# Kernel optimization log

Hardware: AMD Instinct MI355X
Metric: run time of the kernel (lower is better)

Reference implementation:

```python
import jax, jax.numpy as jnp
import numpy as np

TOP_K_FREQ = 16


def setup_inputs() -> dict:
    key = jax.random.key(0)
    x = jax.random.normal(key, (64, 4096, 128), dtype=jnp.float32)
    return {"x": x}


def reference(x):
    B, L, C = x.shape
    freq = jnp.fft.rfft(x, axis=1)              # [B, F, C] complex, F = L//2 + 1
    F = freq.shape[1]
    k = min(TOP_K_FREQ, F)
    mag = jnp.abs(freq)                          # [B, F, C]
    # top-k over frequency axis, vectorized across (B, C)
    mag_bcf = jnp.transpose(mag, (0, 2, 1))      # [B, C, F]
    _, idx = jax.lax.top_k(mag_bcf, k)           # idx: [B, C, k]
    b_ix = jnp.arange(B)[:, None, None]
    c_ix = jnp.arange(C)[None, :, None]
    mask_bcf = jnp.zeros((B, C, F), dtype=x.dtype).at[b_ix, c_ix, idx].set(1.0)
    mask = jnp.transpose(mask_bcf, (0, 2, 1))    # [B, F, C]
    freq_filtered = freq * mask
    out = jnp.fft.irfft(freq_filtered, n=L, axis=1)  # [B, L, C]
    return out.astype(x.dtype)
```

## Files before the change

kernel.cpp:

```cpp
#include <hip/hip_runtime.h>


#define SWZ(i) ((i) ^ (((i) >> 4) & 15))

__device__ __forceinline__ int drev16(int x) {
  return ((x & 15) << 8) | (x & 0xF0) | ((x >> 8) & 15);
}

__device__ __forceinline__ float2 cmulf(float2 a, float c, float s) {
  return make_float2(a.x * c - a.y * s, a.x * s + a.y * c);
}

__device__ __forceinline__ void bfly4(float2& a0, float2& a1, float2& a2, float2& a3) {
  float ar = a0.x + a2.x, ai = a0.y + a2.y;
  float br = a0.x - a2.x, bi = a0.y - a2.y;
  float cr = a1.x + a3.x, ci = a1.y + a3.y;
  float dr = a1.x - a3.x, di = a1.y - a3.y;
  a0 = make_float2(ar + cr, ai + ci);
  a1 = make_float2(br + di, bi - dr);
  a2 = make_float2(ar - cr, ai - ci);
  a3 = make_float2(br - di, bi + dr);
}

__device__ __forceinline__ void dft16(float2* v) {
  const float C16[10] = {1.f, 0.9238795325112867f, 0.7071067811865476f, 0.3826834323650898f, 0.f,
                         -0.3826834323650898f, -0.7071067811865476f, -0.9238795325112867f, -1.f,
                         -0.9238795325112867f};
  const float S16[10] = {0.f, -0.3826834323650898f, -0.7071067811865476f, -0.9238795325112867f, -1.f,
                         -0.9238795325112867f, -0.7071067811865476f, -0.3826834323650898f, 0.f,
                         0.3826834323650898f};
  #pragma unroll
  for (int j2 = 0; j2 < 4; j2++) {
    bfly4(v[j2], v[j2 + 4], v[j2 + 8], v[j2 + 12]);
    if (j2 > 0) {
      v[j2 + 4]  = cmulf(v[j2 + 4],  C16[j2],     S16[j2]);
      v[j2 + 8]  = cmulf(v[j2 + 8],  C16[2 * j2], S16[2 * j2]);
      v[j2 + 12] = cmulf(v[j2 + 12], C16[3 * j2], S16[3 * j2]);
    }
  }
  #pragma unroll
  for (int r2 = 0; r2 < 4; r2++) bfly4(v[4 * r2], v[4 * r2 + 1], v[4 * r2 + 2], v[4 * r2 + 3]);
}

template <int STRIDE, int M>
__device__ __forceinline__ void fft_pass(float2* Zl, int base, int j) {
  const int kRev4[16] = {0, 4, 8, 12, 1, 5, 9, 13, 2, 6, 10, 14, 3, 7, 11, 15};
  float2 v[16];
  #pragma unroll
  for (int p = 0; p < 16; p++) v[p] = Zl[SWZ(base + j + STRIDE * p)];
  dft16(v);
  #pragma unroll
  for (int r = 0; r < 16; r++) {
    float2 u = v[kRev4[r]];
    if (M > 0 && r > 0) {
      int a = (j * r) & (M - 1);
      float x = (float)a * (1.0f / (float)M);
      float s = -__builtin_amdgcn_sinf(x);
      float c =  __builtin_amdgcn_cosf(x);
      u = cmulf(u, c, s);
    }
    Zl[SWZ(base + j + STRIDE * r)] = u;
  }
}


__global__ __launch_bounds__(256, 4) void fourier_fused(
    const float2* __restrict__ X2, float2* __restrict__ O2) {
  __shared__ float2 Z[4096];
  __shared__ float4 CF[32];
  __shared__ float  CFf[32];

  const int tid = threadIdx.x;
  const int o = ((blockIdx.x & 7) << 9) + (blockIdx.x >> 3);
  const int b = o >> 6;
  const int q = o & 63;

  const float2* src = X2 + (size_t)b * 4096 * 64 + q;
  #pragma unroll
  for (int k = 0; k < 16; k++) {
    int l = tid + 256 * k;
    Z[SWZ(l)] = src[(size_t)l * 64];
  }
  __syncthreads();

  fft_pass<256, 4096>(Z, 0, tid);
  __syncthreads();
  fft_pass<16, 256>(Z, (tid >> 4) << 8, tid & 15);
  __syncthreads();
  fft_pass<1, 0>(Z, tid << 4, 0);
  __syncthreads();

  const int wv = tid >> 6;
  const int lane = tid & 63;

  if (wv < 2) {
    const int ch = wv;
    int rF = 0; float rA = 0.f, rB = 0.f;
    float m2[32];
    #pragma unroll
    for (int k = 0; k < 32; k++) {
      int f = lane + (k << 6);
      float2 P = Z[SWZ(drev16(f))];
      float2 Q = Z[SWZ(drev16((4096 - f) & 4095))];
      float xr = ch ? (P.y + Q.y) : (P.x + Q.x);
      float xi = ch ? (Q.x - P.x) : (P.y - Q.y);
      m2[k] = xr * xr + xi * xi;
    }
    float m2x = -1.f;
    if (lane == 0) {
      float2 P = Z[SWZ(8)];
      float t = ch ? P.y : P.x;
      m2x = 4.f * t * t;
    }
    for (int r = 0; r < 16; r++) {
      float bv = -1e30f; int bf = 0;
      #pragma unroll
      for (int k = 0; k < 32; k++) {
        int f = lane + (k << 6);
        if (m2[k] > bv) { bv = m2[k]; bf = f; }
      }
      if (m2x > bv) { bv = m2x; bf = 2048; }
      #pragma unroll
      for (int off = 32; off; off >>= 1) {
        float ov = __shfl_down(bv, off);
        int   of = __shfl_down(bf, off);
        if (ov > bv || (ov == bv && of < bf)) { bv = ov; bf = of; }
      }
      bf = __shfl(bf, 0);
      if (lane == r) {
        rF = bf;
        float2 P = Z[SWZ(drev16(bf))];
        float2 Q = Z[SWZ(drev16((4096 - bf) & 4095))];
        rA = ch ? 0.5f * (P.y + Q.y) : 0.5f * (P.x + Q.x);
        rB = ch ? 0.5f * (Q.x - P.x) : 0.5f * (P.y - Q.y);
      }
      if (bf == 2048) {
        if (lane == 0) m2x = -2.f;
      } else if ((bf & 63) == lane) {
        int kk = bf >> 6;
        #pragma unroll
        for (int k = 0; k < 32; k++) if (k == kk) m2[k] = -2.f;
      }
    }

    if (lane < 16) {
      const float inv = 2.44140625e-4f;
      float w = (rF == 0 || rF == 2048) ? inv : 2.f * inv;
      float fv = (float)rF;
      float dx = fv * 0.0625f;
      dx -= floorf(dx);
      float cd = __builtin_amdgcn_cosf(dx);
      float sd = __builtin_amdgcn_sinf(dx);
      CF[ch * 16 + lane] = make_float4(w * rA, -w * rB, cd, sd);
      CFf[ch * 16 + lane] = fv;
    }
  }
  __syncthreads();

  float* S = (float*)Z;
  const float tf = (float)tid;
  #pragma unroll
  for (int cc = 0; cc < 2; cc++) {
    float u[16], v[16], T[16];
    #pragma unroll
    for (int j = 0; j < 16; j++) {
      float4 cf = CF[cc * 16 + j];
      float f  = CFf[cc * 16 + j];
      float x0 = f * tf * 2.44140625e-4f;
      x0 -= floorf(x0);
      float c0 = __builtin_amdgcn_cosf(x0);
      float s0 = __builtin_amdgcn_sinf(x0);
      float G = fmaf(cf.x, c0, cf.y * s0);
      float H = fmaf(cf.y, c0, -cf.x * s0);
      u[j] = G;
      v[j] = fmaf(G, cf.z, -H * cf.w);
      T[j] = cf.z + cf.z;
    }
    #pragma unroll
    for (int k = 0; k < 16; k += 2) {
      float s0a = 0.f, s1a = 0.f;
      #pragma unroll
      for (int j = 0; j < 16; j++) {
        s0a += u[j];
        v[j] = fmaf(T[j], u[j], -v[j]);
      }
      #pragma unroll
      for (int j = 0; j < 16; j++) {
        s1a += v[j];
        u[j] = fmaf(T[j], v[j], -u[j]);
      }
      S[cc * 4096 + tid + 256 * k]       = s0a;
      S[cc * 4096 + tid + 256 * (k + 1)] = s1a;
    }
  }

  float2* dst = O2 + (size_t)b * 4096 * 64 + q;
  #pragma unroll
  for (int k = 0; k < 16; k++) {
    int l = tid + 256 * k;
    dst[(size_t)l * 64] = make_float2(S[l], S[4096 + l]);
  }
}

extern "C" void kernel_launch(void* const* d_in, const int* in_sizes, int n_in,
                              void* d_out, int out_size, void* d_ws, size_t ws_size,
                              hipStream_t stream) {
  (void)in_sizes; (void)n_in; (void)ws_size; (void)out_size; (void)d_ws;
  const float2* x = (const float2*)d_in[0];
  float2* out = (float2*)d_out;

  fourier_fused<<<dim3(64 * 64), dim3(256), 0, stream>>>(x, out);
}
```

Measured before the change: 504.7 us.

## Switch to radix-8 FFT with 512 threads per block

Replaces the three-pass radix-16 in-LDS FFT with four radix-8 passes and doubles the block size to 512 threads. Each thread now holds 8 instead of 16 complex values, which lowers register pressure and raises the number of waves resident to hide global-memory latency. The twiddle phase, bit-reversal indexing and synthesis stride are updated to match. It adds one extra LDS pass and barrier per block and more threads idle during the two-wave top-k section.

```diff
diff --git a/kernel.cpp b/kernel.cpp
--- a/kernel.cpp
+++ b/kernel.cpp
@@ -3,68 +3,69 @@
 
 #define SWZ(i) ((i) ^ (((i) >> 4) & 15))
 
-__device__ __forceinline__ int drev16(int x) {
-  return ((x & 15) << 8) | (x & 0xF0) | ((x >> 8) & 15);
+__device__ __forceinline__ int drev8(int x) {
+  return ((x & 7) << 9) | ((x & 0x38) << 3) | ((x >> 3) & 0x38) | ((x >> 9) & 7);
 }
 
 __device__ __forceinline__ float2 cmulf(float2 a, float c, float s) {
   return make_float2(a.x * c - a.y * s, a.x * s + a.y * c);
 }
 
-__device__ __forceinline__ void bfly4(float2& a0, float2& a1, float2& a2, float2& a3) {
-  float ar = a0.x + a2.x, ai = a0.y + a2.y;
-  float br = a0.x - a2.x, bi = a0.y - a2.y;
-  float cr = a1.x + a3.x, ci = a1.y + a3.y;
-  float dr = a1.x - a3.x, di = a1.y - a3.y;
-  a0 = make_float2(ar + cr, ai + ci);
-  a1 = make_float2(br + di, bi - dr);
-  a2 = make_float2(ar - cr, ai - ci);
-  a3 = make_float2(br - di, bi + dr);
-}
-
-__device__ __forceinline__ void dft16(float2* v) {
-  const float C16[10] = {1.f, 0.9238795325112867f, 0.7071067811865476f, 0.3826834323650898f, 0.f,
-                         -0.3826834323650898f, -0.7071067811865476f, -0.9238795325112867f, -1.f,
-                         -0.9238795325112867f};
-  const float S16[10] = {0.f, -0.3826834323650898f, -0.7071067811865476f, -0.9238795325112867f, -1.f,
-                         -0.9238795325112867f, -0.7071067811865476f, -0.3826834323650898f, 0.f,
-                         0.3826834323650898f};
-  #pragma unroll
-  for (int j2 = 0; j2 < 4; j2++) {
-    bfly4(v[j2], v[j2 + 4], v[j2 + 8], v[j2 + 12]);
-    if (j2 > 0) {
-      v[j2 + 4]  = cmulf(v[j2 + 4],  C16[j2],     S16[j2]);
-      v[j2 + 8]  = cmulf(v[j2 + 8],  C16[2 * j2], S16[2 * j2]);
-      v[j2 + 12] = cmulf(v[j2 + 12], C16[3 * j2], S16[3 * j2]);
-    }
-  }
-  #pragma unroll
-  for (int r2 = 0; r2 < 4; r2++) bfly4(v[4 * r2], v[4 * r2 + 1], v[4 * r2 + 2], v[4 * r2 + 3]);
+__device__ __forceinline__ float2 cadd(float2 a, float2 b) { return make_float2(a.x + b.x, a.y + b.y); }
+__device__ __forceinline__ float2 csub(float2 a, float2 b) { return make_float2(a.x - b.x, a.y - b.y); }
+__device__ __forceinline__ float2 cmulnegi(float2 a) { return make_float2(a.y, -a.x); }
+__device__ __forceinline__ float2 cmulposi(float2 a) { return make_float2(-a.y, a.x); }
+
+__device__ __forceinline__ void dft8(float2* a) {
+  const float R = 0.7071067811865476f;
+  float2 t0 = cadd(a[0], a[4]), t1 = cadd(a[1], a[5]);
+  float2 t2 = cadd(a[2], a[6]), t3 = cadd(a[3], a[7]);
+  float2 u0 = csub(a[0], a[4]);
+  float2 d1 = csub(a[1], a[5]);
+  float2 u1 = make_float2(R * (d1.x + d1.y), R * (d1.y - d1.x));
+  float2 u2 = cmulnegi(csub(a[2], a[6]));
+  float2 d3 = csub(a[3], a[7]);
+  float2 u3 = make_float2(R * (d3.y - d3.x), R * (-(d3.x + d3.y)));
+  {
+    float2 b0 = cadd(t0, t2), b1 = csub(t0, t2);
+    float2 b2 = cadd(t1, t3), b3 = csub(t1, t3);
+    a[0] = cadd(b0, b2);
+    a[2] = cadd(b1, cmulnegi(b3));
+    a[4] = csub(b0, b2);
+    a[6] = cadd(b1, cmulposi(b3));
+  }
+  {
+    float2 b0 = cadd(u0, u2), b1 = csub(u0, u2);
+    float2 b2 = cadd(u1, u3), b3 = csub(u1, u3);
+    a[1] = cadd(b0, b2);
+    a[3] = cadd(b1, cmulnegi(b3));
+    a[5] = csub(b0, b2);
+    a[7] = cadd(b1, cmulposi(b3));
+  }
 }
 
 template <int STRIDE, int M>
-__device__ __forceinline__ void fft_pass(float2* Zl, int base, int j) {
-  const int kRev4[16] = {0, 4, 8, 12, 1, 5, 9, 13, 2, 6, 10, 14, 3, 7, 11, 15};
-  float2 v[16];
-  #pragma unroll
-  for (int p = 0; p < 16; p++) v[p] = Zl[SWZ(base + j + STRIDE * p)];
-  dft16(v);
-  #pragma unroll
-  for (int r = 0; r < 16; r++) {
-    float2 u = v[kRev4[r]];
-    if (M > 0 && r > 0) {
-      int a = (j * r) & (M - 1);
+__device__ __forceinline__ void fft_pass8(float2* Zl, int base, int j) {
+  float2 v[8];
+  #pragma unroll
+  for (int p = 0; p < 8; p++) v[p] = Zl[SWZ(base + j + STRIDE * p)];
+  dft8(v);
+  #pragma unroll
+  for (int r = 1; r < 8; r++) {
+    if (M > 8) {
+      int a = j * r;
       float x = (float)a * (1.0f / (float)M);
       float s = -__builtin_amdgcn_sinf(x);
       float c =  __builtin_amdgcn_cosf(x);
-      u = cmulf(u, c, s);
-    }
-    Zl[SWZ(base + j + STRIDE * r)] = u;
-  }
-}
-
-
-__global__ __launch_bounds__(256, 4) void fourier_fused(
+      v[r] = cmulf(v[r], c, s);
+    }
+  }
+  #pragma unroll
+  for (int r = 0; r < 8; r++) Zl[SWZ(base + j + STRIDE * r)] = v[r];
+}
+
+
+__global__ __launch_bounds__(512, 8) void fourier_fused(
     const float2* __restrict__ X2, float2* __restrict__ O2) {
   __shared__ float2 Z[4096];
   __shared__ float4 CF[32];
@@ -77,17 +78,19 @@
 
   const float2* src = X2 + (size_t)b * 4096 * 64 + q;
   #pragma unroll
-  for (int k = 0; k < 16; k++) {
-    int l = tid + 256 * k;
+  for (int k = 0; k < 8; k++) {
+    int l = tid + 512 * k;
     Z[SWZ(l)] = src[(size_t)l * 64];
   }
   __syncthreads();
 
-  fft_pass<256, 4096>(Z, 0, tid);
-  __syncthreads();
-  fft_pass<16, 256>(Z, (tid >> 4) << 8, tid & 15);
-  __syncthreads();
-  fft_pass<1, 0>(Z, tid << 4, 0);
+  fft_pass8<512, 4096>(Z, 0, tid);
+  __syncthreads();
+  fft_pass8<64, 512>(Z, (tid >> 6) << 9, tid & 63);
+  __syncthreads();
+  fft_pass8<8, 64>(Z, (tid >> 3) << 6, tid & 7);
+  __syncthreads();
+  fft_pass8<1, 8>(Z, tid << 3, 0);
   __syncthreads();
 
   const int wv = tid >> 6;
@@ -100,15 +103,15 @@
     #pragma unroll
     for (int k = 0; k < 32; k++) {
       int f = lane + (k << 6);
-      float2 P = Z[SWZ(drev16(f))];
-      float2 Q = Z[SWZ(drev16((4096 - f) & 4095))];
+      float2 P = Z[SWZ(drev8(f))];
+      float2 Q = Z[SWZ(drev8((4096 - f) & 4095))];
       float xr = ch ? (P.y + Q.y) : (P.x + Q.x);
       float xi = ch ? (Q.x - P.x) : (P.y - Q.y);
       m2[k] = xr * xr + xi * xi;
     }
     float m2x = -1.f;
     if (lane == 0) {
-      float2 P = Z[SWZ(8)];
+      float2 P = Z[SWZ(4)];
       float t = ch ? P.y : P.x;
       m2x = 4.f * t * t;
     }
@@ -129,8 +132,8 @@
       bf = __shfl(bf, 0);
       if (lane == r) {
         rF = bf;
-        float2 P = Z[SWZ(drev16(bf))];
-        float2 Q = Z[SWZ(drev16((4096 - bf) & 4095))];
+        float2 P = Z[SWZ(drev8(bf))];
+        float2 Q = Z[SWZ(drev8((4096 - bf) & 4095))];
         rA = ch ? 0.5f * (P.y + Q.y) : 0.5f * (P.x + Q.x);
         rB = ch ? 0.5f * (Q.x - P.x) : 0.5f * (P.y - Q.y);
       }
@@ -147,7 +150,7 @@
       const float inv = 2.44140625e-4f;
       float w = (rF == 0 || rF == 2048) ? inv : 2.f * inv;
       float fv = (float)rF;
-      float dx = fv * 0.0625f;
+      float dx = fv * 0.125f;
       dx -= floorf(dx);
       float cd = __builtin_amdgcn_cosf(dx);
       float sd = __builtin_amdgcn_sinf(dx);
@@ -177,7 +180,7 @@
       T[j] = cf.z + cf.z;
     }
     #pragma unroll
-    for (int k = 0; k < 16; k += 2) {
+    for (int k = 0; k < 8; k += 2) {
       float s0a = 0.f, s1a = 0.f;
       #pragma unroll
       for (int j = 0; j < 16; j++) {
@@ -189,15 +192,15 @@
         s1a += v[j];
         u[j] = fmaf(T[j], v[j], -u[j]);
       }
-      S[cc * 4096 + tid + 256 * k]       = s0a;
-      S[cc * 4096 + tid + 256 * (k + 1)] = s1a;
+      S[cc * 4096 + tid + 512 * k]       = s0a;
+      S[cc * 4096 + tid + 512 * (k + 1)] = s1a;
     }
   }
 
   float2* dst = O2 + (size_t)b * 4096 * 64 + q;
   #pragma unroll
-  for (int k = 0; k < 16; k++) {
-    int l = tid + 256 * k;
+  for (int k = 0; k < 8; k++) {
+    int l = tid + 512 * k;
     dst[(size_t)l * 64] = make_float2(S[l], S[4096 + l]);
   }
 }
@@ -209,5 +212,5 @@
   const float2* x = (const float2*)d_in[0];
   float2* out = (float2*)d_out;
 
-  fourier_fused<<<dim3(64 * 64), dim3(256), 0, stream>>>(x, out);
-}
+  fourier_fused<<<dim3(64 * 64), dim3(512), 0, stream>>>(x, out);
+}
```

New measurement: 596.0 us. 1.18x slower.

## Process four channels per block with float4 global loads and stores

Applied to the files above, without the earlier changes.

Each block now handles four channels instead of two. It loads them as float4 and runs two sequential packed-complex FFT and top-k passes, keeping the second pair in registers. The synthesis step is restructured into grouped chunks accumulating 16 outputs, and the results are written back as float4. The intent is wider, better-coalesced global accesses and half as many blocks. The cost is more registers and serialized work per block, which may reduce occupancy.

```diff
diff --git a/kernel.cpp b/kernel.cpp
--- a/kernel.cpp
+++ b/kernel.cpp
@@ -63,109 +63,17 @@
   }
 }
 
-
-__global__ __launch_bounds__(256, 4) void fourier_fused(
-    const float2* __restrict__ X2, float2* __restrict__ O2) {
-  __shared__ float2 Z[4096];
-  __shared__ float4 CF[32];
-  __shared__ float  CFf[32];
-
-  const int tid = threadIdx.x;
-  const int o = ((blockIdx.x & 7) << 9) + (blockIdx.x >> 3);
-  const int b = o >> 6;
-  const int q = o & 63;
-
-  const float2* src = X2 + (size_t)b * 4096 * 64 + q;
-  #pragma unroll
-  for (int k = 0; k < 16; k++) {
-    int l = tid + 256 * k;
-    Z[SWZ(l)] = src[(size_t)l * 64];
-  }
-  __syncthreads();
-
-  fft_pass<256, 4096>(Z, 0, tid);
-  __syncthreads();
-  fft_pass<16, 256>(Z, (tid >> 4) << 8, tid & 15);
-  __syncthreads();
-  fft_pass<1, 0>(Z, tid << 4, 0);
-  __syncthreads();
-
-  const int wv = tid >> 6;
-  const int lane = tid & 63;
-
-  if (wv < 2) {
-    const int ch = wv;
-    int rF = 0; float rA = 0.f, rB = 0.f;
-    float m2[32];
+__device__ __forceinline__ void synthc(const float4* CF, const float* CFf,
+                                       int cbase, float tf, float* acc) {
+  #pragma unroll
+  for (int k = 0; k < 16; k++) acc[k] = 0.f;
+  #pragma unroll 1
+  for (int g = 0; g < 4; g++) {
+    float u[4], v[4], T[4];
     #pragma unroll
-    for (int k = 0; k < 32; k++) {
-      int f = lane + (k << 6);
-      float2 P = Z[SWZ(drev16(f))];
-      float2 Q = Z[SWZ(drev16((4096 - f) & 4095))];
-      float xr = ch ? (P.y + Q.y) : (P.x + Q.x);
-      float xi = ch ? (Q.x - P.x) : (P.y - Q.y);
-      m2[k] = xr * xr + xi * xi;
-    }
-    float m2x = -1.f;
-    if (lane == 0) {
-      float2 P = Z[SWZ(8)];
-      float t = ch ? P.y : P.x;
-      m2x = 4.f * t * t;
-    }
-    for (int r = 0; r < 16; r++) {
-      float bv = -1e30f; int bf = 0;
-      #pragma unroll
-      for (int k = 0; k < 32; k++) {
-        int f = lane + (k << 6);
-        if (m2[k] > bv) { bv = m2[k]; bf = f; }
-      }
-      if (m2x > bv) { bv = m2x; bf = 2048; }
-      #pragma unroll
-      for (int off = 32; off; off >>= 1) {
-        float ov = __shfl_down(bv, off);
-        int   of = __shfl_down(bf, off);
-        if (ov > bv || (ov == bv && of < bf)) { bv = ov; bf = of; }
-      }
-      bf = __shfl(bf, 0);
-      if (lane == r) {
-        rF = bf;
-        float2 P = Z[SWZ(drev16(bf))];
-        float2 Q = Z[SWZ(drev16((4096 - bf) & 4095))];
-        rA = ch ? 0.5f * (P.y + Q.y) : 0.5f * (P.x + Q.x);
-        rB = ch ? 0.5f * (Q.x - P.x) : 0.5f * (P.y - Q.y);
-      }
-      if (bf == 2048) {
-        if (lane == 0) m2x = -2.f;
-      } else if ((bf & 63) == lane) {
-        int kk = bf >> 6;
-        #pragma unroll
-        for (int k = 0; k < 32; k++) if (k == kk) m2[k] = -2.f;
-      }
-    }
-
-    if (lane < 16) {
-      const float inv = 2.44140625e-4f;
-      float w = (rF == 0 || rF == 2048) ? inv : 2.f * inv;
-      float fv = (float)rF;
-      float dx = fv * 0.0625f;
-      dx -= floorf(dx);
-      float cd = __builtin_amdgcn_cosf(dx);
-      float sd = __builtin_amdgcn_sinf(dx);
-      CF[ch * 16 + lane] = make_float4(w * rA, -w * rB, cd, sd);
-      CFf[ch * 16 + lane] = fv;
-    }
-  }
-  __syncthreads();
-
-  float* S = (float*)Z;
-  const float tf = (float)tid;
-  #pragma unroll
-  for (int cc = 0; cc < 2; cc++) {
-    float u[16], v[16], T[16];
-    #pragma unroll
-    for (int j = 0; j < 16; j++) {
-      float4 cf = CF[cc * 16 + j];
-      float f  = CFf[cc * 16 + j];
+    for (int j = 0; j < 4; j++) {
+      float4 cf = CF[cbase + g * 4 + j];
+      float f  = CFf[cbase + g * 4 + j];
       float x0 = f * tf * 2.44140625e-4f;
       x0 -= floorf(x0);
       float c0 = __builtin_amdgcn_cosf(x0);
@@ -178,27 +86,134 @@
     }
     #pragma unroll
     for (int k = 0; k < 16; k += 2) {
-      float s0a = 0.f, s1a = 0.f;
-      #pragma unroll
-      for (int j = 0; j < 16; j++) {
-        s0a += u[j];
-        v[j] = fmaf(T[j], u[j], -v[j]);
-      }
-      #pragma unroll
-      for (int j = 0; j < 16; j++) {
-        s1a += v[j];
-        u[j] = fmaf(T[j], v[j], -u[j]);
-      }
-      S[cc * 4096 + tid + 256 * k]       = s0a;
-      S[cc * 4096 + tid + 256 * (k + 1)] = s1a;
-    }
-  }
-
-  float2* dst = O2 + (size_t)b * 4096 * 64 + q;
+      #pragma unroll
+      for (int j = 0; j < 4; j++) { acc[k] += u[j];     v[j] = fmaf(T[j], u[j], -v[j]); }
+      #pragma unroll
+      for (int j = 0; j < 4; j++) { acc[k + 1] += v[j]; u[j] = fmaf(T[j], v[j], -u[j]); }
+    }
+  }
+}
+
+
+__global__ __launch_bounds__(256, 4) void fourier_fused(
+    const float4* __restrict__ X4, float4* __restrict__ O4) {
+  __shared__ float2 Z[4096];
+  __shared__ float4 CF[64];
+  __shared__ float  CFf[64];
+
+  const int tid = threadIdx.x;
+  const int wv = tid >> 6;
+  const int lane = tid & 63;
+  const int o = ((blockIdx.x & 7) << 8) + (blockIdx.x >> 3);
+  const int b = o >> 5;
+  const int q = o & 31;
+
+  const float inv = 2.44140625e-4f;
+  const float4* src = X4 + (size_t)b * 4096 * 32 + q;
+
+  float pr[16], pi[16];
   #pragma unroll
   for (int k = 0; k < 16; k++) {
     int l = tid + 256 * k;
-    dst[(size_t)l * 64] = make_float2(S[l], S[4096 + l]);
+    float4 v = src[(size_t)l * 32];
+    Z[SWZ(l)] = make_float2(v.x, v.y);
+    pr[k] = v.z;
+    pi[k] = v.w;
+  }
+  __syncthreads();
+
+  #pragma unroll 1
+  for (int half = 0; half < 2; half++) {
+    if (half) {
+      #pragma unroll
+      for (int k = 0; k < 16; k++) Z[SWZ(tid + 256 * k)] = make_float2(pr[k], pi[k]);
+      __syncthreads();
+    }
+
+    fft_pass<256, 4096>(Z, 0, tid);
+    __syncthreads();
+    fft_pass<16, 256>(Z, (tid >> 4) << 8, tid & 15);
+    __syncthreads();
+    fft_pass<1, 0>(Z, tid << 4, 0);
+    __syncthreads();
+
+    if (wv < 2) {
+      const int ch = wv;
+      float m2[32];
+      #pragma unroll
+      for (int k = 0; k < 32; k++) {
+        int f = lane + (k << 6);
+        float2 P = Z[SWZ(drev16(f))];
+        float2 Q = Z[SWZ(drev16((4096 - f) & 4095))];
+        float xr = ch ? (P.y + Q.y) : (P.x + Q.x);
+        float xi = ch ? (Q.x - P.x) : (P.y - Q.y);
+        m2[k] = xr * xr + xi * xi;
+      }
+      float m2x = -1.f;
+      if (lane == 0) {
+        float2 P = Z[SWZ(8)];
+        float t = ch ? P.y : P.x;
+        m2x = 4.f * t * t;
+      }
+      for (int r = 0; r < 16; r++) {
+        float bv = -1e30f; int bf = 0;
+        #pragma unroll
+        for (int k = 0; k < 32; k++) {
+          int f = lane + (k << 6);
+          if (m2[k] > bv) { bv = m2[k]; bf = f; }
+        }
+        if (m2x > bv) { bv = m2x; bf = 2048; }
+        #pragma unroll
+        for (int off = 32; off; off >>= 1) {
+          float ov = __shfl_down(bv, off);
+          int   of = __shfl_down(bf, off);
+          if (ov > bv || (ov == bv && of < bf)) { bv = ov; bf = of; }
+        }
+        bf = __shfl(bf, 0);
+        if (lane == r) {
+          float fv = (float)bf;
+          float2 P = Z[SWZ(drev16(bf))];
+          float2 Q = Z[SWZ(drev16((4096 - bf) & 4095))];
+          float rA = ch ? 0.5f * (P.y + Q.y) : 0.5f * (P.x + Q.x);
+          float rB = ch ? 0.5f * (Q.x - P.x) : 0.5f * (P.y - Q.y);
+          float w = (bf == 0 || bf == 2048) ? inv : 2.f * inv;
+          float dx = fv * 0.0625f;
+          dx -= floorf(dx);
+          float cd = __builtin_amdgcn_cosf(dx);
+          float sd = __builtin_amdgcn_sinf(dx);
+          int gc = half * 2 + ch;
+          CF[gc * 16 + r] = make_float4(w * rA, -w * rB, cd, sd);
+          CFf[gc * 16 + r] = fv;
+        }
+        if (bf == 2048) {
+          if (lane == 0) m2x = -2.f;
+        } else if ((bf & 63) == lane) {
+          int kk = bf >> 6;
+          #pragma unroll
+          for (int k = 0; k < 32; k++) if (k == kk) m2[k] = -2.f;
+        }
+      }
+    }
+    __syncthreads();
+  }
+
+  float* Zf = (float*)Z;
+  float acc[16], acc2[16], acc3[16];
+  const float tf = (float)tid;
+  synthc(CF, CFf, 0, tf, acc);
+  #pragma unroll
+  for (int k = 0; k < 16; k++) Zf[tid + 256 * k] = acc[k];
+  synthc(CF, CFf, 16, tf, acc);
+  #pragma unroll
+  for (int k = 0; k < 16; k++) Zf[4096 + tid + 256 * k] = acc[k];
+  synthc(CF, CFf, 32, tf, acc2);
+  synthc(CF, CFf, 48, tf, acc3);
+
+  float4* dst = O4 + (size_t)b * 4096 * 32 + q;
+  #pragma unroll
+  for (int k = 0; k < 16; k++) {
+    int l = tid + 256 * k;
+    dst[(size_t)l * 32] = make_float4(Zf[l], Zf[4096 + l], acc2[k], acc3[k]);
   }
 }
 
@@ -206,8 +221,8 @@
                               void* d_out, int out_size, void* d_ws, size_t ws_size,
                               hipStream_t stream) {
   (void)in_sizes; (void)n_in; (void)ws_size; (void)out_size; (void)d_ws;
-  const float2* x = (const float2*)d_in[0];
-  float2* out = (float2*)d_out;
-
-  fourier_fused<<<dim3(64 * 64), dim3(256), 0, stream>>>(x, out);
-}
+  const float4* x = (const float4*)d_in[0];
+  float4* out = (float4*)d_out;
+
+  fourier_fused<<<dim3(64 * 32), dim3(256), 0, stream>>>(x, out);
+}
```

New measurement: 831.4 us. 1.65x slower.
